# Performance work log

Hardware: AMD Instinct MI355X
Metric: run time of the kernel (lower is better)

## Reference

```python
import jax, jax.numpy as jnp
import numpy as np

N_HEADS = 16
HEAD_K = 128
HEAD_V = 128
SCALE_BASE = 512.0
THETA_BASE = 10000.0


def xpos_tables(seq_len, head_size):
    # Faithful to the torch xpos module with start=0, end=seq_len (no cache)
    alpha = 0.4 * head_size
    drange = np.arange(2, head_size + 2, 2, dtype=np.float32)
    theta = np.repeat((1.0 / THETA_BASE) ** (drange / head_size), 2)  # [head_size]
    zeta = np.repeat((drange / (head_size / 2) + alpha) / (1 + alpha), 2)  # [head_size]
    half = seq_len // 2
    seq = (np.arange(-half, seq_len - half, dtype=np.float32) / SCALE_BASE)[:, None, None]  # [S,1,1]
    c = np.cos(seq * theta[None, None, :])  # [S,1,head_size]
    s = np.sin(seq * theta[None, None, :])
    t = zeta[None, None, :] ** seq
    return jnp.asarray(c), jnp.asarray(s), jnp.asarray(t), jnp.asarray(1.0 / t)


def rotate_every_two(x):
    return jnp.stack((-x[..., 1::2], x[..., 0::2]), axis=-1).reshape(x.shape)


def setup_inputs() -> dict:
    key = jax.random.key(0)
    ks = jax.random.split(key, 5)
    B, S, E = 2, 2048, 2048
    return {
        "activations": jax.random.normal(ks[0], (B, S, E), dtype=jnp.float32),
        "Wq": 0.02 * jax.random.normal(ks[1], (N_HEADS * HEAD_K, E), dtype=jnp.float32),
        "Wk": 0.02 * jax.random.normal(ks[2], (N_HEADS * HEAD_K, E), dtype=jnp.float32),
        "Wv": 0.02 * jax.random.normal(ks[3], (N_HEADS * HEAD_V, E), dtype=jnp.float32),
        "Wo": 0.02 * jax.random.normal(ks[4], (E, N_HEADS * HEAD_V), dtype=jnp.float32),
    }


def reference(activations, Wq, Wk, Wv, Wo):
    B, S, E = activations.shape
    # QKV projections (torch Linear: y = x @ W.T), split heads
    q = (activations @ Wq.T).reshape(B, S, N_HEADS, HEAD_K)
    k = (activations @ Wk.T).reshape(B, S, N_HEADS, HEAD_K)
    v = (activations @ Wv.T).reshape(B, S, N_HEADS, HEAD_V)
    # xpos rotary + scale; tables have shape [S,1,head] broadcasting over heads
    c, s, t, invt = xpos_tables(S, HEAD_K)
    q = (q * c + rotate_every_two(q) * s) * t
    k = (k * c + rotate_every_two(k) * s) * invt
    # causal scaled dot-product attention
    scale = 1.0 / jnp.sqrt(jnp.float32(HEAD_K))
    scores = jnp.einsum("bqhd,bkhd->bhqk", q, k) * scale  # [B,H,S,S]
    causal = jnp.tril(jnp.ones((S, S), dtype=bool))
    scores = jnp.where(causal, scores, jnp.float32(-1e30))
    probs = jax.nn.softmax(scores, axis=-1)
    out = jnp.einsum("bhqk,bkhd->bqhd", probs, v).reshape(B, S, N_HEADS * HEAD_V)
    # down projection (dropout_rate=0 / eval mode)
    return out @ Wo.T
```

## Files before the change

### kernel.cpp

```cpp
#include <hip/hip_runtime.h>
#include <hip/hip_bf16.h>

typedef __attribute__((ext_vector_type(8))) short bf16x8;
typedef __attribute__((ext_vector_type(4))) float f32x4;
typedef __attribute__((ext_vector_type(4))) _Float16 f16x4;
typedef __attribute__((ext_vector_type(8))) _Float16 f16x8;
typedef __attribute__((ext_vector_type(4))) unsigned short u16x4;

#define B_ 2
#define S_ 2048
#define E_ 2048
#define H_ 16
#define D_ 128
#define ELEMS (B_*S_*E_)
#define WELEMS (E_*E_)

__device__ __forceinline__ unsigned short f2bf(float x) {
  unsigned int u = __float_as_uint(x);
  u += 0x7fffu + ((u >> 16) & 1u);
  return (unsigned short)(u >> 16);
}

__device__ __forceinline__ void async_load16(const void* g, void* l) {
  __builtin_amdgcn_global_load_lds(
      (const __attribute__((address_space(1))) unsigned int*)g,
      (__attribute__((address_space(3))) unsigned int*)l, 16, 0, 0);
}

__global__ __launch_bounds__(256)
void cvt_f32_bf16(const float* __restrict__ src, unsigned short* __restrict__ dst, int n4)
{
  const int i = blockIdx.x * 256 + threadIdx.x;
  if (i < n4) {
    const f32x4 v = ((const f32x4*)src)[i];
    u16x4 o;
    o.x = f2bf(v.x); o.y = f2bf(v.y); o.z = f2bf(v.z); o.w = f2bf(v.w);
    ((u16x4*)dst)[i] = o;
  }
}

__global__ __launch_bounds__(256)
void cvt4_f32_bf16(const float* __restrict__ s0, const float* __restrict__ s1,
                   const float* __restrict__ s2, const float* __restrict__ s3,
                   unsigned short* __restrict__ d0, unsigned short* __restrict__ d1,
                   unsigned short* __restrict__ d2, unsigned short* __restrict__ d3,
                   int n4)
{
  const int i = blockIdx.x * 256 + threadIdx.x;
  if (i >= n4) return;
  const float* s; unsigned short* d;
  switch (blockIdx.y) {
    case 0: s = s0; d = d0; break;
    case 1: s = s1; d = d1; break;
    case 2: s = s2; d = d2; break;
    default: s = s3; d = d3; break;
  }
  const f32x4 v = ((const f32x4*)s)[i];
  u16x4 o;
  o.x = f2bf(v.x); o.y = f2bf(v.y); o.z = f2bf(v.z); o.w = f2bf(v.w);
  ((u16x4*)d)[i] = o;
}

template<int OUTMODE>
__global__ __launch_bounds__(512, 2)
void gemm_ring3(const __hip_bfloat16* __restrict__ A,
                const __hip_bfloat16* __restrict__ Bw,
                void* __restrict__ C, int M, int N, int K)
{
  extern __shared__ char lds[];
  const int lane = threadIdx.x & 63;
  const int w    = threadIdx.x >> 6;
  const int fr   = lane & 15;
  const int fg   = lane >> 4;

  const int nblk = N >> 7;
  const int cpx  = gridDim.x >> 3;
  const int lin  = blockIdx.x;
  const int swz  = (lin & 7) * cpx + (lin >> 3);
  const int m0 = (swz / nblk) << 8;
  const int n0 = (swz % nblk) << 7;

  const int Ssw = (fg ^ ((fr >> 1) & 3)) << 4;
  const int pA  = ((w >> 1) * 64 + fr) * 64 + Ssw;
  const int pB  = 32768 + ((w & 1) * 64 + fr) * 64 + Ssw;

  const int srow = w * 16 + (lane >> 2);
  const int ks   = ((lane & 3) ^ ((lane >> 3) & 3)) * 8;
  const __hip_bfloat16* Asrc = A  + (size_t)(m0 + srow) * K + ks;
  const __hip_bfloat16* Bsrc = Bw + (size_t)(n0 + srow) * K + ks;
  const int dstA = srow * 64 + (lane & 3) * 16;

#define STG(NB, KH, KT) do {                                                   \
    const size_t ko_ = (size_t)(KT)*64 + (KH)*32;                              \
    async_load16(Asrc + ko_,                                                   \
                 lds + (NB)*49152 + (KH)*16384 + dstA);                        \
    async_load16(Asrc + (size_t)128*K + ko_,                                   \
                 lds + (NB)*49152 + (KH)*16384 + 8192 + dstA);                 \
    async_load16(Bsrc + ko_,                                                   \
                 lds + (NB)*49152 + 32768 + (KH)*8192 + dstA);                 \
  } while (0)

#define RD(AR, BR, KK, BB) do {                                                \
    const char* pa_ = lds + (BB)*49152 + (KK)*16384 + pA;                      \
    AR[0] = *(const bf16x8*)(pa_);        AR[1] = *(const bf16x8*)(pa_ + 1024);\
    AR[2] = *(const bf16x8*)(pa_ + 2048); AR[3] = *(const bf16x8*)(pa_ + 3072);\
    const char* pb_ = lds + (BB)*49152 + (KK)*8192 + pB;                       \
    BR[0] = *(const bf16x8*)(pb_);        BR[1] = *(const bf16x8*)(pb_ + 1024);\
    BR[2] = *(const bf16x8*)(pb_ + 2048); BR[3] = *(const bf16x8*)(pb_ + 3072);\
  } while (0)

#define MFMA16(AR, BR)                                                         \
    _Pragma("unroll")                                                          \
    for (int i_ = 0; i_ < 4; i_++)                                             \
    _Pragma("unroll")                                                          \
    for (int j_ = 0; j_ < 4; j_++)                                             \
      acc[i_][j_] = __builtin_amdgcn_mfma_f32_16x16x32_bf16(                   \
          AR[i_], BR[j_], acc[i_][j_], 0, 0, 0)

#define BARX() __builtin_amdgcn_s_barrier()
#define LGKM0() do { asm volatile("s_waitcnt lgkmcnt(0)" ::: "memory");        \
                     __builtin_amdgcn_sched_barrier(0); } while (0)
#define VMW(NN) asm volatile("s_waitcnt vmcnt(" #NN ")" ::: "memory")
#define PRIO(P) __builtin_amdgcn_s_setprio(P)

  f32x4 acc[4][4];
#pragma unroll
  for (int i = 0; i < 4; i++)
#pragma unroll
    for (int j = 0; j < 4; j++) acc[i][j] = (f32x4)0.0f;

  bf16x8 a0[4], b0[4], a1[4], b1[4];

  STG(0, 0, 0);
  STG(0, 1, 0);
  STG(1, 0, 1);
  STG(1, 1, 1);
  VMW(6);
  BARX();

  const int nk = K >> 6;
  int bb = 0;
  for (int t = 0; t < nk; ++t) {
    const int nb = (bb == 0) ? 2 : bb - 1;
    const bool stg = (t + 2) < nk;
    RD(a0, b0, 0, bb);
    if (stg) STG(nb, 0, t + 2);
    BARX(); LGKM0();
    PRIO(1); MFMA16(a0, b0); PRIO(0);
    RD(a1, b1, 1, bb);
    if (stg) STG(nb, 1, t + 2);
    LGKM0();
    PRIO(1); MFMA16(a1, b1); PRIO(0);
    if (stg) { VMW(6); } else { VMW(0); }
    BARX();
    bb = (bb == 2) ? 0 : bb + 1;
  }

  const int wr = (w >> 1) * 64, wc = (w & 1) * 64;
#pragma unroll
  for (int mi = 0; mi < 4; mi++) {
    const int row = m0 + wr + mi*16 + fg*4;
#pragma unroll
    for (int nj = 0; nj < 4; nj++) {
      const int col = n0 + wc + nj*16 + fr;
#pragma unroll
      for (int r = 0; r < 4; r++) {
        if (OUTMODE == 1) {
          ((float*)C)[(size_t)(row + r)*N + col] = acc[mi][nj][r];
        } else if (OUTMODE == 0) {
          ((unsigned short*)C)[(size_t)(row + r)*N + col] = f2bf(acc[mi][nj][r]);
        } else if (OUTMODE == 2) {
          const int rr = row + r;
          const int b = rr >> 11, s = rr & 2047;
          const int h = col >> 7, d = col & 127;
          ((unsigned short*)C)[(((size_t)(b*H_ + h) << 11) + s)*D_ + d] = f2bf(acc[mi][nj][r]);
        } else {
          const int rr = row + r;
          const int b = rr >> 11, s = rr & 2047;
          const int t2 = col >> 11;
          const int h = (col >> 7) & 15, d = col & 127;
          ((unsigned short*)C)[(size_t)t2*ELEMS +
              (((size_t)(b*H_ + h) << 11) + s)*D_ + d] = f2bf(acc[mi][nj][r]);
        }
      }
    }
  }
#undef STG
#undef RD
#undef MFMA16
#undef BARX
#undef LGKM0
#undef VMW
#undef PRIO
}

__global__ __launch_bounds__(256)
void xpos_rotary(__hip_bfloat16* __restrict__ Q, __hip_bfloat16* __restrict__ Kt)
{
  const int idx = blockIdx.x * 256 + threadIdx.x;
  const int j = idx & 63;
  const int s = (idx >> 6) & 2047;
  const float seq = (float)(s - 1024) * (1.0f/512.0f);
  const float dr = 2.0f + 2.0f*(float)j;
  const float theta = expf(dr * (1.0f/128.0f) * -9.210340371976184f);
  const float zeta  = (dr * (1.0f/64.0f) + 51.2f) * (1.0f/52.2f);
  const float ang = seq * theta;
  const float c  = cosf(ang);
  const float sn = sinf(ang);
  const float t  = expf(seq * logf(zeta));
  const float it = 1.0f / t;

  const size_t base = (size_t)(idx >> 6) * 128 + 2*j;
  unsigned short* Qs = (unsigned short*)Q;
  unsigned short* Ks = (unsigned short*)Kt;
  const float q0 = __bfloat162float(Q[base]),  q1 = __bfloat162float(Q[base+1]);
  Qs[base]   = f2bf((q0*c - q1*sn) * t);
  Qs[base+1] = f2bf((q1*c + q0*sn) * t);
  const float k0 = __bfloat162float(Kt[base]), k1 = __bfloat162float(Kt[base+1]);
  Ks[base]   = f2bf((k0*c - k1*sn) * it);
  Ks[base+1] = f2bf((k1*c + k0*sn) * it);
}

__global__ __launch_bounds__(256)
void transpose_v(const __hip_bfloat16* __restrict__ Vh, _Float16* __restrict__ VT3)
{
  __shared__ float tile[32][33];
  const int tx = threadIdx.x, ty = threadIdx.y;
  const int bh = blockIdx.z;
  const int s0 = blockIdx.x * 32, d0 = blockIdx.y * 32;
  const int kt = s0 >> 6, koff = s0 & 63;
#pragma unroll
  for (int r = 0; r < 4; r++) {
    const int s = s0 + ty + r*8;
    tile[ty + r*8][tx] = __bfloat162float(Vh[((size_t)bh*S_ + s)*D_ + d0 + tx]);
  }
  __syncthreads();
  const int key = koff + tx;
  const int g = (key >> 2) & 3, rr = key & 3, half = (key >> 5) & 1, s1 = (key >> 4) & 1;
  const size_t base = (size_t)bh*S_*D_ + (size_t)kt*8192 + g*16 + half*8 + s1*4 + rr;
#pragma unroll
  for (int r = 0; r < 4; r++) {
    const int d = d0 + ty + r*8;
    VT3[base + d*64] = (_Float16)tile[tx][ty + r*8];
  }
}

__global__ __launch_bounds__(256, 2)
void attn_fwd(const __hip_bfloat16* __restrict__ Qh,
              const __hip_bfloat16* __restrict__ Kh,
              const _Float16* __restrict__ VT3,
              __hip_bfloat16* __restrict__ O)
{
  __shared__ union {
    struct { unsigned short Kt[2][4096]; _Float16 Vt[2][4096]; } st;
    float ep[64*132];
  } sh;

  const int lane = threadIdx.x & 63;
  const int w    = threadIdx.x >> 6;
  const int L  = blockIdx.x;
  const int bh = (L & 7) + 8*((L >> 3) & 3);
  const int x  = 31 - (L >> 5);
  const int b = bh >> 4, h = bh & 15;
  const int q0 = x*64 + w*16;
  const int qc = lane & 15;
  const int g  = lane >> 4;
  const int qv = q0 + qc;

  const __hip_bfloat16* Kb = Kh + (size_t)bh*S_*D_;
  const _Float16* vtb = VT3 + (size_t)bh*S_*D_;

  const int kswz  = (qc & 7) << 4;
  const int vbase = qc*64 + ((g ^ ((qc >> 1) & 3)) << 4);

#define STAGE(BUF, P) do {                                                       \
    const int kb0_ = (P)*32;                                                     \
    _Pragma("unroll")                                                            \
    for (int ii = 0; ii < 2; ii++) {                                             \
      const int chunk = w*2 + ii;                                                \
      const int key   = chunk*4 + (lane >> 4);                                   \
      const int srcin = ((lane & 15)*16) ^ ((key & 7) << 4);                     \
      async_load16((const char*)Kb + (size_t)(kb0_ + key)*256 + srcin,           \
                   (char*)sh.st.Kt[BUF] + chunk*1024);                           \
    }                                                                            \
    const int kt_ = (P) >> 1, h_ = (P) & 1;                                      \
    _Pragma("unroll")                                                            \
    for (int ii = 0; ii < 2; ii++) {                                             \
      const int chunk = w*2 + ii;                                                \
      const int dd = chunk*16 + (lane >> 2);                                     \
      const int gg = (lane & 3) ^ ((lane >> 3) & 3);                             \
      async_load16((const char*)vtb + ((size_t)kt_*8192 + dd*64 + gg*16 + h_*8)*2,\
                   (char*)sh.st.Vt[BUF] + chunk*1024);                           \
    }                                                                            \
  } while (0)

#define COMPUTE(BUF, P) do {                                                     \
    const int k0_ = (P)*32;                                                      \
    const char* Kl = (const char*)sh.st.Kt[BUF];                                 \
    const char* Vl = (const char*)sh.st.Vt[BUF];                                 \
    bf16x8 ka[4], kbb[4]; f16x8 vv[8];                                           \
    _Pragma("unroll")                                                            \
    for (int c = 0; c < 4; c++) {                                                \
      const int off = (c*64 + g*16) ^ kswz;                                      \
      ka[c]  = *(const bf16x8*)(Kl + qc*256 + off);                              \
      kbb[c] = *(const bf16x8*)(Kl + (16 + qc)*256 + off);                       \
    }                                                                            \
    _Pragma("unroll")                                                            \
    for (int t = 0; t < 8; t++) vv[t] = *(const f16x8*)(Vl + t*1024 + vbase);    \
    f32x4 sA = (f32x4)0.0f, sB = (f32x4)0.0f;                                    \
    _Pragma("unroll")                                                            \
    for (int c = 0; c < 4; c++) {                                                \
      sA = __builtin_amdgcn_mfma_f32_16x16x32_bf16(ka[c],  qf[c], sA, 0, 0, 0);  \
      sB = __builtin_amdgcn_mfma_f32_16x16x32_bf16(kbb[c], qf[c], sB, 0, 0, 0);  \
    }                                                                            \
    float sv[8];                                                                 \
    _Pragma("unroll")                                                            \
    for (int r = 0; r < 4; r++) {                                                \
      sv[r]   = (k0_      + g*4 + r <= qv) ? sA[r]*scale : -1e30f;               \
      sv[4+r] = (k0_ + 16 + g*4 + r <= qv) ? sB[r]*scale : -1e30f;               \
    }                                                                            \
    float mx = sv[0];                                                            \
    _Pragma("unroll")                                                            \
    for (int j = 1; j < 8; j++) mx = fmaxf(mx, sv[j]);                           \
    mx = fmaxf(mx, __shfl_xor(mx, 16));                                          \
    mx = fmaxf(mx, __shfl_xor(mx, 32));                                          \
    const float m_new = fmaxf(m_i, mx);                                          \
    const float alpha = __expf(m_i - m_new);                                     \
    float p[8], ps = 0.0f;                                                       \
    _Pragma("unroll")                                                            \
    for (int j = 0; j < 8; j++) { p[j] = __expf(sv[j] - m_new); ps += p[j]; }    \
    ps += __shfl_xor(ps, 16);                                                    \
    ps += __shfl_xor(ps, 32);                                                    \
    l_i = l_i*alpha + ps;                                                        \
    m_i = m_new;                                                                 \
    f16x4 pA, pB;                                                                \
    _Pragma("unroll")                                                            \
    for (int r = 0; r < 4; r++) { pA[r] = (_Float16)p[r]; pB[r] = (_Float16)p[4+r]; } \
    _Pragma("unroll")                                                            \
    for (int t = 0; t < 8; t++) acc_o[t] *= alpha;                               \
    _Pragma("unroll")                                                            \
    for (int t = 0; t < 8; t++) {                                                \
      const f16x4 vA = __builtin_shufflevector(vv[t], vv[t], 0, 1, 2, 3);        \
      const f16x4 vB = __builtin_shufflevector(vv[t], vv[t], 4, 5, 6, 7);        \
      acc_o[t] = __builtin_amdgcn_mfma_f32_16x16x16f16(vA, pA, acc_o[t], 0, 0, 0); \
      acc_o[t] = __builtin_amdgcn_mfma_f32_16x16x16f16(vB, pB, acc_o[t], 0, 0, 0); \
    }                                                                            \
  } while (0)

  STAGE(0, 0);

  bf16x8 qf[4];
  {
    const __hip_bfloat16* qrow = Qh + ((size_t)bh*S_ + qv)*D_ + g*8;
#pragma unroll
    for (int c = 0; c < 4; c++) qf[c] = *(const bf16x8*)(qrow + c*32);
  }

  f32x4 acc_o[8];
#pragma unroll
  for (int t = 0; t < 8; t++) acc_o[t] = (f32x4)0.0f;
  float m_i = -1e30f, l_i = 0.0f;
  const float scale = 0.08838834764831845f;

  const int ntile = 2*x + 2;

  __syncthreads();

  for (int p = 0; p < ntile; ++p) {
    if (p + 1 < ntile) STAGE((p + 1) & 1, p + 1);
    COMPUTE(p & 1, p);
    __syncthreads();
  }

  const float inv_l = 1.0f / l_i;
#pragma unroll
  for (int t = 0; t < 8; t++)
#pragma unroll
    for (int r = 0; r < 4; r++)
      sh.ep[(w*16 + qc)*132 + t*16 + g*4 + r] = acc_o[t][r] * inv_l;
  __syncthreads();

  const int row = threadIdx.x >> 2;
  const int c0  = (threadIdx.x & 3) * 32;
  unsigned short* Os = (unsigned short*)O;
  const size_t obase = ((size_t)b*S_ + x*64 + row)*E_ + h*D_;
#pragma unroll
  for (int i = 0; i < 8; i++) {
    const f32x4 v4 = *(const f32x4*)(sh.ep + row*132 + c0 + i*4);
    u16x4 o4;
    o4.x = f2bf(v4.x); o4.y = f2bf(v4.y); o4.z = f2bf(v4.z); o4.w = f2bf(v4.w);
    *(u16x4*)(Os + obase + c0 + i*4) = o4;
  }
#undef STAGE
#undef COMPUTE
}

extern "C" void kernel_launch(void* const* d_in, const int* in_sizes, int n_in,
                              void* d_out, int out_size, void* d_ws, size_t ws_size,
                              hipStream_t stream)
{
  (void)in_sizes; (void)n_in; (void)out_size; (void)ws_size;
  const float* act = (const float*)d_in[0];
  const float* Wq  = (const float*)d_in[1];
  const float* Wk  = (const float*)d_in[2];
  const float* Wv  = (const float*)d_in[3];
  const float* Wo  = (const float*)d_in[4];

  __hip_bfloat16* actb = (__hip_bfloat16*)d_ws;
  __hip_bfloat16* Wqb  = actb + ELEMS;
  __hip_bfloat16* Wkb  = Wqb + WELEMS;
  __hip_bfloat16* Wvb  = Wkb + WELEMS;
  __hip_bfloat16* Wob  = Wvb + WELEMS;
  __hip_bfloat16* Q    = Wob + WELEMS;
  __hip_bfloat16* Kp   = Q + ELEMS;
  __hip_bfloat16* V    = Kp + ELEMS;
  _Float16*       VT   = (_Float16*)(V + ELEMS);
  __hip_bfloat16* AO   = V;

  cvt_f32_bf16<<<ELEMS/4/256, 256, 0, stream>>>(act, (unsigned short*)actb, ELEMS/4);
  cvt4_f32_bf16<<<dim3(WELEMS/4/256, 4), 256, 0, stream>>>(
      Wq, Wk, Wv, Wo,
      (unsigned short*)Wqb, (unsigned short*)Wkb,
      (unsigned short*)Wvb, (unsigned short*)Wob, WELEMS/4);

  gemm_ring3<3><<<(B_*S_/256)*(3*E_/128), 512, 147456, stream>>>(
      actb, Wqb, Q, B_*S_, 3*E_, E_);

  xpos_rotary<<<(B_*S_*H_*64)/256, 256, 0, stream>>>(Q, Kp);
  transpose_v<<<dim3(S_/32, D_/32, B_*H_), dim3(32, 8), 0, stream>>>(V, VT);
  attn_fwd<<<1024, 256, 0, stream>>>(Q, Kp, VT, AO);

  gemm_ring3<1><<<(B_*S_/256)*(E_/128), 512, 147456, stream>>>(
      AO, Wob, d_out, B_*S_, E_, E_);
}
```

Baseline: 402.6 us.

## Restructure GEMM main loop: unroll triple-buffer ring, merge LDS reads, drop mid barrier

The bf16 GEMM main loop is unrolled by three so the ring-buffer indices become compile-time constants. Global source pointers are advanced incrementally instead of recomputed each step. Each K-tile now issues both LDS fragment reads up front, then all async loads, then 32 MFMAs back to back. The intermediate barrier and the explicit lgkmcnt waits are removed, cutting synchronisation per tile, but this relies on the compiler inserting correct waits and increases register pressure from holding both fragment sets at once.

```diff
diff --git a/kernel.cpp b/kernel.cpp
--- a/kernel.cpp
+++ b/kernel.cpp
@@ -63,9 +63,9 @@
 
 template<int OUTMODE>
 __global__ __launch_bounds__(512, 2)
-void gemm_ring3(const __hip_bfloat16* __restrict__ A,
-                const __hip_bfloat16* __restrict__ Bw,
-                void* __restrict__ C, int M, int N, int K)
+void gemm_p4(const __hip_bfloat16* __restrict__ A,
+             const __hip_bfloat16* __restrict__ Bw,
+             void* __restrict__ C, int M, int N, int K)
 {
   extern __shared__ char lds[];
   const int lane = threadIdx.x & 63;
@@ -86,19 +86,21 @@
 
   const int srow = w * 16 + (lane >> 2);
   const int ks   = ((lane & 3) ^ ((lane >> 3) & 3)) * 8;
-  const __hip_bfloat16* Asrc = A  + (size_t)(m0 + srow) * K + ks;
-  const __hip_bfloat16* Bsrc = Bw + (size_t)(n0 + srow) * K + ks;
+  const __hip_bfloat16* Asrc  = A  + (size_t)(m0 + srow) * K + ks;
+  const __hip_bfloat16* A2src = Asrc + (size_t)128 * K;
+  const __hip_bfloat16* Bsrc  = Bw + (size_t)(n0 + srow) * K + ks;
   const int dstA = srow * 64 + (lane & 3) * 16;
 
-#define STG(NB, KH, KT) do {                                                   \
-    const size_t ko_ = (size_t)(KT)*64 + (KH)*32;                              \
-    async_load16(Asrc + ko_,                                                   \
-                 lds + (NB)*49152 + (KH)*16384 + dstA);                        \
-    async_load16(Asrc + (size_t)128*K + ko_,                                   \
-                 lds + (NB)*49152 + (KH)*16384 + 8192 + dstA);                 \
-    async_load16(Bsrc + ko_,                                                   \
-                 lds + (NB)*49152 + 32768 + (KH)*8192 + dstA);                 \
+#define STG(NB) do {                                                           \
+    async_load16(Asrc,       lds + (NB)*49152 +                 dstA);         \
+    async_load16(Asrc + 32,  lds + (NB)*49152 + 16384 +         dstA);         \
+    async_load16(A2src,      lds + (NB)*49152 +          8192 + dstA);         \
+    async_load16(A2src + 32, lds + (NB)*49152 + 16384 +  8192 + dstA);         \
+    async_load16(Bsrc,       lds + (NB)*49152 + 32768 +         dstA);         \
+    async_load16(Bsrc + 32,  lds + (NB)*49152 + 32768 +  8192 + dstA);         \
   } while (0)
+
+#define ADV() do { Asrc += 64; A2src += 64; Bsrc += 64; } while (0)
 
 #define RD(AR, BR, KK, BB) do {                                                \
     const char* pa_ = lds + (BB)*49152 + (KK)*16384 + pA;                      \
@@ -117,12 +119,21 @@
       acc[i_][j_] = __builtin_amdgcn_mfma_f32_16x16x32_bf16(                   \
           AR[i_], BR[j_], acc[i_][j_], 0, 0, 0)
 
-#define BARX() __builtin_amdgcn_s_barrier()
-#define LGKM0() do { asm volatile("s_waitcnt lgkmcnt(0)" ::: "memory");        \
-                     __builtin_amdgcn_sched_barrier(0); } while (0)
+#define SB0()  __builtin_amdgcn_sched_barrier(0)
+#define BARX() do { __builtin_amdgcn_s_barrier(); SB0(); } while (0)
 #define VMW(NN) asm volatile("s_waitcnt vmcnt(" #NN ")" ::: "memory")
 #define PRIO(P) __builtin_amdgcn_s_setprio(P)
 
+#define TILE(BB, NB, T) do {                                                   \
+    const bool stg_ = (T) + 2 < nk;                                            \
+    RD(a0, b0, 0, BB);                                                         \
+    RD(a1, b1, 1, BB);                                                         \
+    if (stg_) { STG(NB); ADV(); }                                              \
+    PRIO(1); MFMA16(a0, b0); MFMA16(a1, b1); PRIO(0);                          \
+    if (stg_) { VMW(6); } else { VMW(0); }                                     \
+    BARX();                                                                    \
+  } while (0)
+
   f32x4 acc[4][4];
 #pragma unroll
   for (int i = 0; i < 4; i++)
@@ -131,30 +142,21 @@
 
   bf16x8 a0[4], b0[4], a1[4], b1[4];
 
-  STG(0, 0, 0);
-  STG(0, 1, 0);
-  STG(1, 0, 1);
-  STG(1, 1, 1);
+  const int nk = K >> 6;
+
+  STG(0); ADV();
+  STG(1); ADV();
   VMW(6);
   BARX();
 
-  const int nk = K >> 6;
-  int bb = 0;
-  for (int t = 0; t < nk; ++t) {
-    const int nb = (bb == 0) ? 2 : bb - 1;
-    const bool stg = (t + 2) < nk;
-    RD(a0, b0, 0, bb);
-    if (stg) STG(nb, 0, t + 2);
-    BARX(); LGKM0();
-    PRIO(1); MFMA16(a0, b0); PRIO(0);
-    RD(a1, b1, 1, bb);
-    if (stg) STG(nb, 1, t + 2);
-    LGKM0();
-    PRIO(1); MFMA16(a1, b1); PRIO(0);
-    if (stg) { VMW(6); } else { VMW(0); }
-    BARX();
-    bb = (bb == 2) ? 0 : bb + 1;
-  }
+  int t = 0;
+  for (; t + 3 <= nk; t += 3) {
+    TILE(0, 2, t);
+    TILE(1, 0, t + 1);
+    TILE(2, 1, t + 2);
+  }
+  if (t < nk) { TILE(0, 2, t); ++t; }
+  if (t < nk) { TILE(1, 0, t); ++t; }
 
   const int wr = (w >> 1) * 64, wc = (w & 1) * 64;
 #pragma unroll
@@ -186,12 +188,14 @@
     }
   }
 #undef STG
+#undef ADV
 #undef RD
 #undef MFMA16
+#undef SB0
 #undef BARX
-#undef LGKM0
 #undef VMW
 #undef PRIO
+#undef TILE
 }
 
 __global__ __launch_bounds__(256)
@@ -423,13 +427,13 @@
       (unsigned short*)Wqb, (unsigned short*)Wkb,
       (unsigned short*)Wvb, (unsigned short*)Wob, WELEMS/4);
 
-  gemm_ring3<3><<<(B_*S_/256)*(3*E_/128), 512, 147456, stream>>>(
+  gemm_p4<3><<<(B_*S_/256)*(3*E_/128), 512, 147456, stream>>>(
       actb, Wqb, Q, B_*S_, 3*E_, E_);
 
   xpos_rotary<<<(B_*S_*H_*64)/256, 256, 0, stream>>>(Q, Kp);
   transpose_v<<<dim3(S_/32, D_/32, B_*H_), dim3(32, 8), 0, stream>>>(V, VT);
   attn_fwd<<<1024, 256, 0, stream>>>(Q, Kp, VT, AO);
 
-  gemm_ring3<1><<<(B_*S_/256)*(E_/128), 512, 147456, stream>>>(
+  gemm_p4<1><<<(B_*S_/256)*(E_/128), 512, 147456, stream>>>(
       AO, Wob, d_out, B_*S_, E_, E_);
 }
```

After: 373.2 us. 1.08x faster.
